# Kernel tuning notes

Measured on AMD Instinct MI355X. Metric: run time of the kernel, lower is better.

Reference implementation:

```python
import jax, jax.numpy as jnp
import numpy as np

SIGMA_COLOR = 0.1
SIGMA_SPATIAL = 5.0
RADIUS = 8


def setup_inputs() -> dict:
    key = jax.random.key(0)
    images = jax.random.uniform(key, (16, 3, 768, 768), dtype=jnp.float32)
    return {"images": images}


def _spatial_affinity(h, w):
    # coordinates of each cell in the (h, w) feature grid, flattened to N = h*w
    y = jnp.repeat(jnp.arange(h, dtype=jnp.float32), w)  # [N]
    x = jnp.tile(jnp.arange(w, dtype=jnp.float32), h)    # [N]
    y_diff = y[:, None] - y[None, :]                      # [N, N]
    x_diff = x[:, None] - x[None, :]                      # [N, N]
    spatial_dist = y_diff ** 2 + x_diff ** 2
    aff = jnp.exp(-spatial_dist / (2.0 * SIGMA_SPATIAL ** 2))
    mask = (jnp.abs(y_diff) <= RADIUS) & (jnp.abs(x_diff) <= RADIUS)
    return aff * mask.astype(aff.dtype)                   # [N, N]


def reference(images):
    B, C, H, W = images.shape
    h, w = H // 16, W // 16
    N = h * w
    # bilinear resize, half-pixel centers == torch align_corners=False
    img_r = jax.image.resize(images, (B, C, h, w), method="bilinear", antialias=False)
    feats = img_r.reshape(B, C, N).transpose(0, 2, 1)     # [B, N, C]
    # ||f_i - f_j||^2 = |f_i|^2 + |f_j|^2 - 2 f_i . f_j  (avoids [B,N,N,C] diff tensor)
    sq = jnp.sum(feats * feats, axis=-1)                  # [B, N]
    dots = jnp.einsum("bic,bjc->bij", feats, feats)       # [B, N, N]
    color_dist = jnp.maximum(sq[:, :, None] + sq[:, None, :] - 2.0 * dots, 0.0)
    color_aff = jnp.exp(-color_dist / (2.0 * SIGMA_COLOR ** 2))  # [B, N, N]
    spatial_aff = _spatial_affinity(h, w)                 # [N, N]
    return color_aff * spatial_aff[None, :, :]            # [B, N, N]
```

## Files before the change

kernel.cpp:

```cpp
#include <hip/hip_runtime.h>

#define BATCH 16
#define CH    3
#define HIN   768
#define WIN   768
#define HS    48
#define WS    48
#define NPIX  (HS * WS)
#define QPR   (NPIX / 4)

__global__ void downsample_kernel(const float* __restrict__ img,
                                  float4* __restrict__ feats) {
    int idx = blockIdx.x * blockDim.x + threadIdx.x;
    if (idx >= BATCH * NPIX) return;
    int b = idx / NPIX;
    int n = idx - b * NPIX;
    int y = n / WS;
    int x = n - y * WS;
    int iy = 16 * y + 7;
    int ix = 16 * x + 7;
    const float* base = img + (size_t)b * CH * HIN * WIN;
    float f[3];
#pragma unroll
    for (int c = 0; c < 3; ++c) {
        const float* p = base + (size_t)c * HIN * WIN;
        const float* r0 = p + (size_t)iy * WIN + ix;
        const float* r1 = r0 + WIN;
        f[c] = 0.25f * (r0[0] + r0[1] + r1[0] + r1[1]);
    }
    feats[idx] = make_float4(f[0], f[1], f[2], 0.0f);
}

__global__ __launch_bounds__(576) void row_affinity_kernel(const float4* __restrict__ feats,
                                                           float4* __restrict__ out) {
    int i = blockIdx.x;
    int b = blockIdx.y;
    int yi = i / WS;
    int xi = i - yi * WS;
    const float4* frow = feats + (size_t)b * NPIX;

    int xq = threadIdx.x;
    int yj = threadIdx.y;
    int dy = yi - yj;

    float4 res;
    if (dy > 8 || dy < -8) {
        res = make_float4(0.f, 0.f, 0.f, 0.f);
    } else {
        float4 fi = frow[i];
        float sdy = (float)(dy * dy);
        int xj0 = xq * 4;
        int j0  = yj * WS + xj0;
        float v[4];
#pragma unroll
        for (int k = 0; k < 4; ++k) {
            int dx = xi - (xj0 + k);
            float4 fj = frow[j0 + k];
            float d0 = fi.x - fj.x;
            float d1 = fi.y - fj.y;
            float d2 = fi.z - fj.z;
            float cd = d0 * d0 + d1 * d1 + d2 * d2;
            float sd = sdy + (float)(dx * dx);
            float e  = __expf(-50.0f * cd - 0.02f * sd);
            v[k] = (dx > 8 || dx < -8) ? 0.0f : e;
        }
        res = make_float4(v[0], v[1], v[2], v[3]);
    }
    out[(size_t)(b * NPIX + i) * QPR + yj * 12 + xq] = res;
}

extern "C" void kernel_launch(void* const* d_in, const int* in_sizes, int n_in,
                              void* d_out, int out_size, void* d_ws, size_t ws_size,
                              hipStream_t stream) {
    const float* img = (const float*)d_in[0];
    float4* feats = (float4*)d_ws;
    float4* out4  = (float4*)d_out;

    {
        int threads = BATCH * NPIX;
        int block = 256;
        int grid = (threads + block - 1) / block;
        downsample_kernel<<<grid, block, 0, stream>>>(img, feats);
    }
    {
        dim3 grid(NPIX, BATCH);
        dim3 block(12, 48);
        row_affinity_kernel<<<grid, block, 0, stream>>>(feats, out4);
    }
}
```

Before: 385.3 us.

## Process a full image row of output pixels per block, reusing neighbor features

```diff
diff --git a/kernel.cpp b/kernel.cpp
--- a/kernel.cpp
+++ b/kernel.cpp
@@ -33,40 +33,47 @@
 
 __global__ __launch_bounds__(576) void row_affinity_kernel(const float4* __restrict__ feats,
                                                            float4* __restrict__ out) {
-    int i = blockIdx.x;
-    int b = blockIdx.y;
-    int yi = i / WS;
-    int xi = i - yi * WS;
-    const float4* frow = feats + (size_t)b * NPIX;
-
+    int yi = blockIdx.x;
+    int b  = blockIdx.y;
     int xq = threadIdx.x;
     int yj = threadIdx.y;
     int dy = yi - yj;
 
-    float4 res;
+    const float4* frow = feats + (size_t)b * NPIX;
+    float4* oquad = out + ((size_t)b * NPIX + (size_t)yi * WS) * QPR + yj * 12 + xq;
+
     if (dy > 8 || dy < -8) {
-        res = make_float4(0.f, 0.f, 0.f, 0.f);
+        const float4 z = make_float4(0.f, 0.f, 0.f, 0.f);
+#pragma unroll 4
+        for (int xi = 0; xi < WS; ++xi) {
+            oquad[(size_t)xi * QPR] = z;
+        }
     } else {
-        float4 fi = frow[i];
-        float sdy = (float)(dy * dy);
         int xj0 = xq * 4;
         int j0  = yj * WS + xj0;
-        float v[4];
+        float4 fj[4];
 #pragma unroll
-        for (int k = 0; k < 4; ++k) {
-            int dx = xi - (xj0 + k);
-            float4 fj = frow[j0 + k];
-            float d0 = fi.x - fj.x;
-            float d1 = fi.y - fj.y;
-            float d2 = fi.z - fj.z;
-            float cd = d0 * d0 + d1 * d1 + d2 * d2;
-            float sd = sdy + (float)(dx * dx);
-            float e  = __expf(-50.0f * cd - 0.02f * sd);
-            v[k] = (dx > 8 || dx < -8) ? 0.0f : e;
+        for (int k = 0; k < 4; ++k) fj[k] = frow[j0 + k];
+        float sdy = (float)(dy * dy);
+        int ibase = yi * WS;
+#pragma unroll 2
+        for (int xi = 0; xi < WS; ++xi) {
+            float4 fi = frow[ibase + xi];
+            float v[4];
+#pragma unroll
+            for (int k = 0; k < 4; ++k) {
+                int dx = xi - (xj0 + k);
+                float d0 = fi.x - fj[k].x;
+                float d1 = fi.y - fj[k].y;
+                float d2 = fi.z - fj[k].z;
+                float cd = d0 * d0 + d1 * d1 + d2 * d2;
+                float sd = sdy + (float)(dx * dx);
+                float e  = __expf(-50.0f * cd - 0.02f * sd);
+                v[k] = (dx > 8 || dx < -8) ? 0.0f : e;
+            }
+            oquad[(size_t)xi * QPR] = make_float4(v[0], v[1], v[2], v[3]);
         }
-        res = make_float4(v[0], v[1], v[2], v[3]);
     }
-    out[(size_t)(b * NPIX + i) * QPR + yj * 12 + xq] = res;
 }
 
 extern "C" void kernel_launch(void* const* d_in, const int* in_sizes, int n_in,
@@ -83,7 +90,7 @@
         downsample_kernel<<<grid, block, 0, stream>>>(img, feats);
     }
     {
-        dim3 grid(NPIX, BATCH);
+        dim3 grid(HS, BATCH);
         dim3 block(12, 48);
         row_affinity_kernel<<<grid, block, 0, stream>>>(feats, out4);
     }
```

Measured after the change: 398.9 us. 1.04x slower.
